# Performance work log

Measured on AMD Instinct MI355X. Metric: run time of the kernel, lower is better.

Reference implementation:

```python
import jax, jax.numpy as jnp
import numpy as np
from jax.ops import segment_sum

N = 100_000     # num nodes
E = 1_600_000   # num edges
G = 1024        # num graphs in batch
DIN, H, EMB, L = 128, 128, 64, 3
EPS = 1e-5


def setup_inputs() -> dict:
    key = jax.random.key(0)
    ks = jax.random.split(key, 12)
    x = jax.random.normal(ks[0], (N, DIN), dtype=jnp.float32)
    edge_index = jax.random.randint(ks[1], (2, E), 0, N, dtype=jnp.int32)
    batch = jnp.sort(jax.random.randint(ks[2], (N,), 0, G, dtype=jnp.int32))
    s = 0.05
    W_in = jax.random.normal(ks[3], (DIN, H), dtype=jnp.float32) * s
    b_in = jnp.zeros((H,), dtype=jnp.float32)
    Ws = jax.random.normal(ks[4], (L, H, H), dtype=jnp.float32) * s
    bs = jnp.zeros((L, H), dtype=jnp.float32)
    gammas = jnp.ones((L, H), dtype=jnp.float32)
    betas = jnp.zeros((L, H), dtype=jnp.float32)
    W1 = jax.random.normal(ks[5], (H, H), dtype=jnp.float32) * s
    b1 = jnp.zeros((H,), dtype=jnp.float32)
    W2 = jax.random.normal(ks[6], (H, EMB), dtype=jnp.float32) * s
    b2 = jnp.zeros((EMB,), dtype=jnp.float32)
    return {"x": x, "edge_index": edge_index, "batch": batch,
            "W_in": W_in, "b_in": b_in, "Ws": Ws, "bs": bs,
            "gammas": gammas, "betas": betas,
            "W1": W1, "b1": b1, "W2": W2, "b2": b2}


def reference(x, edge_index, batch, W_in, b_in, Ws, bs, gammas, betas, W1, b1, W2, b2):
    src, dst = edge_index[0], edge_index[1]
    # GCN normalization with implicit self-loops: deg = in-degree + 1
    deg = segment_sum(jnp.ones((E,), x.dtype), dst, num_segments=N) + 1.0
    dinv = jax.lax.rsqrt(deg)                      # deg^{-1/2}, [N]
    edge_norm = (dinv[src] * dinv[dst])[:, None]   # [E,1]
    self_norm = (dinv * dinv)[:, None]             # [N,1] = 1/deg

    h = jax.nn.relu(x @ W_in + b_in)               # input projection (dropout=0 / eval)
    for i in range(L):
        hw = h @ Ws[i]                             # [N,H] linear transform
        agg = segment_sum(hw[src] * edge_norm, dst, num_segments=N)
        h = agg + hw * self_norm + bs[i]           # GCNConv output (self-loop term fused)
        # BatchNorm1d over node dim (training-mode batch statistics)
        mean = jnp.mean(h, axis=0)
        var = jnp.var(h, axis=0)
        h = (h - mean) * jax.lax.rsqrt(var + EPS) * gammas[i] + betas[i]
        h = jax.nn.relu(h)

    # global mean pool per graph
    cnt = segment_sum(jnp.ones((N,), x.dtype), batch, num_segments=G)
    pooled = segment_sum(h, batch, num_segments=G) / jnp.maximum(cnt, 1.0)[:, None]

    out = jax.nn.relu(pooled @ W1 + b1) @ W2 + b2  # [G, EMB]
    return out
```

## Files before the change

### kernel.cpp

```cpp
#include <hip/hip_runtime.h>

#define HD 128
#define EMB 64
#define EPS 1e-5f

__device__ __forceinline__ float4 ld4(const float* p) {
    return *reinterpret_cast<const float4*>(p);
}

__device__ __forceinline__ unsigned short f2bf(float f) {
    unsigned u = __float_as_uint(f);
    u += 0x7FFF + ((u >> 16) & 1);
    return (unsigned short)(u >> 16);
}
__device__ __forceinline__ float bf2f(unsigned short b) {
    return __uint_as_float((unsigned)b << 16);
}
__device__ __forceinline__ float blo(unsigned u) { return __uint_as_float(u << 16); }
__device__ __forceinline__ float bhi(unsigned u) { return __uint_as_float(u & 0xffff0000u); }

__global__ void k_hist(const int* __restrict__ dst, int* __restrict__ deg, int e) {
    int i = blockIdx.x * blockDim.x + threadIdx.x;
    if (i < e) atomicAdd(&deg[dst[i]], 1);
}

__global__ void k_dinv(const int* __restrict__ deg, float* __restrict__ dinv, int n) {
    int i = blockIdx.x * blockDim.x + threadIdx.x;
    if (i < n) dinv[i] = 1.0f / sqrtf((float)deg[i] + 1.0f);
}

__global__ void k_scan_part(const int* __restrict__ deg, int* __restrict__ out,
                            int* __restrict__ bsum, int n) {
    __shared__ int s[256];
    int i = blockIdx.x * 256 + threadIdx.x;
    int v = (i < n) ? deg[i] : 0;
    s[threadIdx.x] = v;
    __syncthreads();
    #pragma unroll
    for (int off = 1; off < 256; off <<= 1) {
        int t = (threadIdx.x >= off) ? s[threadIdx.x - off] : 0;
        __syncthreads();
        s[threadIdx.x] += t;
        __syncthreads();
    }
    if (i < n) out[i] = s[threadIdx.x] - v;
    if (threadIdx.x == 255) bsum[blockIdx.x] = s[255];
}

__global__ void k_scan_mid(int* __restrict__ bsum, int nb) {
    __shared__ int s[512];
    int t = threadIdx.x;
    int v = (t < nb) ? bsum[t] : 0;
    s[t] = v;
    __syncthreads();
    for (int off = 1; off < 512; off <<= 1) {
        int u = (t >= off) ? s[t - off] : 0;
        __syncthreads();
        s[t] += u;
        __syncthreads();
    }
    if (t < nb) bsum[t] = s[t] - v;
}

__global__ void k_scan_add(int* __restrict__ rs, const int* __restrict__ bsum,
                           int n, int e_total) {
    int i = blockIdx.x * 256 + threadIdx.x;
    if (i < n) rs[i] += bsum[blockIdx.x];
    if (i == 0) rs[n] = e_total;
}

__global__ void k_scatter(const int* __restrict__ src, const int* __restrict__ dst,
                          int* __restrict__ cursor, int* __restrict__ csr_src, int e) {
    int i = blockIdx.x * blockDim.x + threadIdx.x;
    if (i < e) {
        int d = dst[i];
        int pos = atomicAdd(&cursor[d], 1);
        csr_src[pos] = src[i];
    }
}

template <bool APPLY_BN, bool OUT_BIAS_RELU, bool OUT_BF16>
__global__ void k_gemm(const float* __restrict__ A, const float* __restrict__ W,
                       const float* __restrict__ bias,
                       const float* __restrict__ aff_a, const float* __restrict__ aff_b,
                       void* __restrict__ Cout, int M) {
    __shared__ float As[32][64];
    __shared__ float Bs[32][128];
    const int tid = threadIdx.x;
    const int tx = tid & 31;
    const int ty = tid >> 5;
    const int row0 = blockIdx.x * 64;

    float acc[8][4];
    #pragma unroll
    for (int i = 0; i < 8; ++i)
        #pragma unroll
        for (int j = 0; j < 4; ++j) acc[i][j] = 0.0f;

    for (int k0 = 0; k0 < HD; k0 += 32) {
        #pragma unroll
        for (int it = 0; it < 2; ++it) {
            int idx = tid + it * 256;
            int m = idx >> 3;
            int k4 = (idx & 7) << 2;
            int gm = row0 + m;
            float4 v = make_float4(0.f, 0.f, 0.f, 0.f);
            if (gm < M) v = ld4(A + (size_t)gm * HD + k0 + k4);
            if (APPLY_BN) {
                float4 a4 = ld4(aff_a + k0 + k4);
                float4 b4 = ld4(aff_b + k0 + k4);
                v.x = fmaxf(fmaf(v.x, a4.x, b4.x), 0.f);
                v.y = fmaxf(fmaf(v.y, a4.y, b4.y), 0.f);
                v.z = fmaxf(fmaf(v.z, a4.z, b4.z), 0.f);
                v.w = fmaxf(fmaf(v.w, a4.w, b4.w), 0.f);
            }
            As[k4 + 0][m] = v.x; As[k4 + 1][m] = v.y;
            As[k4 + 2][m] = v.z; As[k4 + 3][m] = v.w;
        }
        #pragma unroll
        for (int it = 0; it < 4; ++it) {
            int idx = tid + it * 256;
            int kk = idx >> 5;
            int n4 = (idx & 31) << 2;
            *reinterpret_cast<float4*>(&Bs[kk][n4]) = ld4(W + (size_t)(k0 + kk) * HD + n4);
        }
        __syncthreads();
        #pragma unroll
        for (int k = 0; k < 32; ++k) {
            float4 b4 = *reinterpret_cast<const float4*>(&Bs[k][tx * 4]);
            float4 a0 = *reinterpret_cast<const float4*>(&As[k][ty * 8]);
            float4 a1 = *reinterpret_cast<const float4*>(&As[k][ty * 8 + 4]);
            float a[8] = {a0.x, a0.y, a0.z, a0.w, a1.x, a1.y, a1.z, a1.w};
            float b[4] = {b4.x, b4.y, b4.z, b4.w};
            #pragma unroll
            for (int i = 0; i < 8; ++i)
                #pragma unroll
                for (int j = 0; j < 4; ++j)
                    acc[i][j] = fmaf(a[i], b[j], acc[i][j]);
        }
        __syncthreads();
    }
    #pragma unroll
    for (int i = 0; i < 8; ++i) {
        int gm = row0 + ty * 8 + i;
        if (gm < M) {
            float4 o = make_float4(acc[i][0], acc[i][1], acc[i][2], acc[i][3]);
            if (OUT_BIAS_RELU) {
                float4 bb = ld4(bias + tx * 4);
                o.x = fmaxf(o.x + bb.x, 0.f);
                o.y = fmaxf(o.y + bb.y, 0.f);
                o.z = fmaxf(o.z + bb.z, 0.f);
                o.w = fmaxf(o.w + bb.w, 0.f);
            }
            if (OUT_BF16) {
                unsigned short b0 = f2bf(o.x), b1 = f2bf(o.y),
                               b2 = f2bf(o.z), b3 = f2bf(o.w);
                uint2 pk;
                pk.x = (unsigned)b0 | ((unsigned)b1 << 16);
                pk.y = (unsigned)b2 | ((unsigned)b3 << 16);
                *reinterpret_cast<uint2*>((unsigned short*)Cout + (size_t)gm * HD + tx * 4) = pk;
            } else {
                *reinterpret_cast<float4*>((float*)Cout + (size_t)gm * HD + tx * 4) = o;
            }
        }
    }
}

#define NPB 8
__global__ void k_agg(const unsigned short* __restrict__ hw, const int* __restrict__ row_start,
                      const int* __restrict__ csr_src, const float* __restrict__ dinv,
                      const float* __restrict__ bias_row, float* __restrict__ h_pre,
                      float* __restrict__ colsum, float* __restrict__ colsumsq, int n) {
    const int tid  = threadIdx.x;
    const int lane = tid & 63;
    const int slot = tid >> 6;
    const int q    = lane & 15;
    const int grp  = lane >> 4;
    const int n0 = blockIdx.x * (4 * NPB);
    const uint4* __restrict__ hw4 = (const uint4*)hw;

    float b8[8];
    #pragma unroll
    for (int k = 0; k < 8; ++k) b8[k] = bias_row[q * 8 + k];

    float psum8[8], psq8[8];
    #pragma unroll
    for (int k = 0; k < 8; ++k) { psum8[k] = 0.f; psq8[k] = 0.f; }

    for (int nn = 0; nn < NPB; ++nn) {
        int node = n0 + nn * 4 + slot;
        if (node >= n) continue;
        float dn = dinv[node];
        float acc[8];
        #pragma unroll
        for (int k = 0; k < 8; ++k) acc[k] = 0.f;

        const int jb = row_start[node], je = row_start[node + 1];
        for (int j = jb; j < je; j += 8) {
            int e0 = j + grp;
            int s0 = (e0 < je) ? csr_src[e0] : 0;
            float w0 = (e0 < je) ? dinv[s0] * dn : 0.f;
            uint4 r0 = hw4[(size_t)s0 * 16 + q];
            int e1 = j + 4 + grp;
            int s1 = (e1 < je) ? csr_src[e1] : 0;
            float w1 = (e1 < je) ? dinv[s1] * dn : 0.f;
            uint4 r1 = hw4[(size_t)s1 * 16 + q];

            acc[0] = fmaf(blo(r0.x), w0, acc[0]); acc[1] = fmaf(bhi(r0.x), w0, acc[1]);
            acc[2] = fmaf(blo(r0.y), w0, acc[2]); acc[3] = fmaf(bhi(r0.y), w0, acc[3]);
            acc[4] = fmaf(blo(r0.z), w0, acc[4]); acc[5] = fmaf(bhi(r0.z), w0, acc[5]);
            acc[6] = fmaf(blo(r0.w), w0, acc[6]); acc[7] = fmaf(bhi(r0.w), w0, acc[7]);

            acc[0] = fmaf(blo(r1.x), w1, acc[0]); acc[1] = fmaf(bhi(r1.x), w1, acc[1]);
            acc[2] = fmaf(blo(r1.y), w1, acc[2]); acc[3] = fmaf(bhi(r1.y), w1, acc[3]);
            acc[4] = fmaf(blo(r1.z), w1, acc[4]); acc[5] = fmaf(bhi(r1.z), w1, acc[5]);
            acc[6] = fmaf(blo(r1.w), w1, acc[6]); acc[7] = fmaf(bhi(r1.w), w1, acc[7]);
        }

        #pragma unroll
        for (int k = 0; k < 8; ++k) acc[k] += __shfl_xor(acc[k], 16, 64);
        #pragma unroll
        for (int k = 0; k < 8; ++k) acc[k] += __shfl_xor(acc[k], 32, 64);

        uint4 ow = hw4[(size_t)node * 16 + q];
        float sn = dn * dn;
        acc[0] = fmaf(blo(ow.x), sn, acc[0] + b8[0]);
        acc[1] = fmaf(bhi(ow.x), sn, acc[1] + b8[1]);
        acc[2] = fmaf(blo(ow.y), sn, acc[2] + b8[2]);
        acc[3] = fmaf(bhi(ow.y), sn, acc[3] + b8[3]);
        acc[4] = fmaf(blo(ow.z), sn, acc[4] + b8[4]);
        acc[5] = fmaf(bhi(ow.z), sn, acc[5] + b8[5]);
        acc[6] = fmaf(blo(ow.w), sn, acc[6] + b8[6]);
        acc[7] = fmaf(bhi(ow.w), sn, acc[7] + b8[7]);

        if (grp == 0) {
            float* dst = h_pre + (size_t)node * HD + q * 8;
            *reinterpret_cast<float4*>(dst)     = make_float4(acc[0], acc[1], acc[2], acc[3]);
            *reinterpret_cast<float4*>(dst + 4) = make_float4(acc[4], acc[5], acc[6], acc[7]);
            #pragma unroll
            for (int k = 0; k < 8; ++k) {
                psum8[k] += acc[k];
                psq8[k] = fmaf(acc[k], acc[k], psq8[k]);
            }
        }
    }

    __shared__ float redS[4][128];
    __shared__ float redQ[4][128];
    if (grp == 0) {
        #pragma unroll
        for (int k = 0; k < 8; ++k) {
            redS[slot][q * 8 + k] = psum8[k];
            redQ[slot][q * 8 + k] = psq8[k];
        }
    }
    __syncthreads();
    int f = tid & 127;
    if (tid < 128) {
        float s = redS[0][f] + redS[1][f] + redS[2][f] + redS[3][f];
        atomicAdd(&colsum[f], s);
    } else {
        float s = redQ[0][f] + redQ[1][f] + redQ[2][f] + redQ[3][f];
        atomicAdd(&colsumsq[f], s);
    }
}

__global__ void k_bncoef(float* __restrict__ colsum, float* __restrict__ colsumsq,
                         const float* __restrict__ gamma, const float* __restrict__ beta,
                         float* __restrict__ aff_a, float* __restrict__ aff_b, int n) {
    int f = threadIdx.x;
    float inv_n = 1.0f / (float)n;
    float mean = colsum[f] * inv_n;
    float var = colsumsq[f] * inv_n - mean * mean;
    float rstd = 1.0f / sqrtf(var + EPS);
    float a = gamma[f] * rstd;
    aff_a[f] = a;
    aff_b[f] = beta[f] - mean * a;
    colsum[f] = 0.f;
    colsumsq[f] = 0.f;
}

__global__ void k_gbounds(const int* __restrict__ batch, int* __restrict__ gstart,
                          int n, int g) {
    int gi = blockIdx.x * blockDim.x + threadIdx.x;
    if (gi > g) return;
    int lo = 0, hi = n;
    while (lo < hi) {
        int mid = (lo + hi) >> 1;
        if (batch[mid] < gi) lo = mid + 1; else hi = mid;
    }
    gstart[gi] = lo;
}

__global__ void k_pool(const float* __restrict__ h_pre, const int* __restrict__ gstart,
                       const float* __restrict__ aff_a, const float* __restrict__ aff_b,
                       float* __restrict__ pooled) {
    const int gi = blockIdx.x;
    const int tid = threadIdx.x;
    const int lane = tid & 63;
    const int half = tid >> 6;
    const float2* __restrict__ h2 = (const float2*)h_pre;
    const float2 a2 = *((const float2*)aff_a + lane);
    const float2 b2 = *((const float2*)aff_b + lane);
    int s = gstart[gi], e = gstart[gi + 1];
    float2 sum = make_float2(0.f, 0.f);
    for (int i = s + half; i < e; i += 2) {
        float2 v = h2[(size_t)i * 64 + lane];
        sum.x += fmaxf(fmaf(v.x, a2.x, b2.x), 0.f);
        sum.y += fmaxf(fmaf(v.y, a2.y, b2.y), 0.f);
    }
    __shared__ float2 red[128];
    red[tid] = sum;
    __syncthreads();
    if (half == 0) {
        float2 o = red[tid + 64];
        sum.x += o.x; sum.y += o.y;
        float inv = 1.0f / fmaxf((float)(e - s), 1.0f);
        float2* p2 = (float2*)pooled;
        p2[(size_t)gi * 64 + lane] = make_float2(sum.x * inv, sum.y * inv);
    }
}

__global__ void k_head(const float* __restrict__ pooled, const float* __restrict__ W1,
                       const float* __restrict__ b1, const float* __restrict__ W2,
                       const float* __restrict__ b2, float* __restrict__ out) {
    __shared__ float p[HD];
    __shared__ float t[HD];
    int gi = blockIdx.x;
    int j = threadIdx.x;
    p[j] = pooled[(size_t)gi * HD + j];
    __syncthreads();
    float acc = b1[j];
    #pragma unroll 8
    for (int k = 0; k < HD; ++k) acc = fmaf(p[k], W1[(size_t)k * HD + j], acc);
    t[j] = fmaxf(acc, 0.f);
    __syncthreads();
    if (j < EMB) {
        float o = b2[j];
        #pragma unroll 8
        for (int k = 0; k < HD; ++k) o = fmaf(t[k], W2[(size_t)k * EMB + j], o);
        out[(size_t)gi * EMB + j] = o;
    }
}

extern "C" void kernel_launch(void* const* d_in, const int* in_sizes, int n_in,
                              void* d_out, int out_size, void* d_ws, size_t ws_size,
                              hipStream_t stream) {
    const float* x     = (const float*)d_in[0];
    const int*   ei    = (const int*)d_in[1];
    const int*   batch = (const int*)d_in[2];
    const float* W_in  = (const float*)d_in[3];
    const float* b_in  = (const float*)d_in[4];
    const float* Ws    = (const float*)d_in[5];
    const float* bs    = (const float*)d_in[6];
    const float* gam   = (const float*)d_in[7];
    const float* bet   = (const float*)d_in[8];
    const float* W1    = (const float*)d_in[9];
    const float* b1    = (const float*)d_in[10];
    const float* W2    = (const float*)d_in[11];
    const float* b2    = (const float*)d_in[12];
    float* out = (float*)d_out;

    const int n = in_sizes[0] / HD;
    const int e = in_sizes[1] / 2;
    const int g = out_size / EMB;

    const int* esrc = ei;
    const int* edst = ei + e;

    char* w = (char*)d_ws;
    auto alloc = [&](size_t bytes) {
        char* p = w;
        w += (bytes + 255) & ~(size_t)255;
        return p;
    };
    float* hbuf             = (float*)alloc((size_t)n * HD * 4);
    unsigned short* hw      = (unsigned short*)alloc((size_t)n * HD * 2);
    int*   csr_src = (int*)alloc((size_t)e * 4);
    int*   deg     = (int*)alloc((size_t)n * 4);
    float* dinv    = (float*)alloc((size_t)n * 4);
    int*   rstart  = (int*)alloc((size_t)(n + 1) * 4);
    int*   cursor  = (int*)alloc((size_t)n * 4);
    int*   bsum    = (int*)alloc(512 * 4);
    float* colsum  = (float*)alloc(256 * 4);
    float* colsumsq = colsum + HD;
    float* aff_a   = (float*)alloc(256 * 4);
    float* aff_b   = aff_a + HD;
    int*   gstart  = (int*)alloc((size_t)(g + 1) * 4);
    float* pooled  = (float*)alloc((size_t)g * HD * 4);

    hipMemsetAsync(deg, 0, (size_t)n * 4, stream);
    hipMemsetAsync(colsum, 0, 256 * 4, stream);

    const int eb = (e + 255) / 256;
    const int nb = (n + 255) / 256;

    k_hist<<<eb, 256, 0, stream>>>(edst, deg, e);
    k_dinv<<<nb, 256, 0, stream>>>(deg, dinv, n);
    k_scan_part<<<nb, 256, 0, stream>>>(deg, rstart, bsum, n);
    k_scan_mid<<<1, 512, 0, stream>>>(bsum, nb);
    k_scan_add<<<nb, 256, 0, stream>>>(rstart, bsum, n, e);
    hipMemcpyAsync(cursor, rstart, (size_t)n * 4, hipMemcpyDeviceToDevice, stream);
    k_scatter<<<eb, 256, 0, stream>>>(esrc, edst, cursor, csr_src, e);

    const int gb = (n + 63) / 64;
    k_gemm<false, true, false><<<gb, 256, 0, stream>>>(x, W_in, b_in, nullptr, nullptr, hbuf, n);

    const int ab = (n + 4 * NPB - 1) / (4 * NPB);
    for (int i = 0; i < 3; ++i) {
        if (i == 0)
            k_gemm<false, false, true><<<gb, 256, 0, stream>>>(
                hbuf, Ws + (size_t)i * HD * HD, nullptr, nullptr, nullptr, hw, n);
        else
            k_gemm<true, false, true><<<gb, 256, 0, stream>>>(
                hbuf, Ws + (size_t)i * HD * HD, nullptr, aff_a, aff_b, hw, n);
        k_agg<<<ab, 256, 0, stream>>>(hw, rstart, csr_src, dinv, bs + (size_t)i * HD,
                                      hbuf, colsum, colsumsq, n);
        k_bncoef<<<1, HD, 0, stream>>>(colsum, colsumsq, gam + (size_t)i * HD,
                                       bet + (size_t)i * HD, aff_a, aff_b, n);
    }

    k_gbounds<<<(g + 256) / 256, 256, 0, stream>>>(batch, gstart, n, g);
    k_pool<<<g, 128, 0, stream>>>(hbuf, gstart, aff_a, aff_b, pooled);
    k_head<<<g, HD, 0, stream>>>(pooled, W1, b1, W2, b2, out);
}
```

Measured before the change: 945.8 us.

## Replace FP32 SIMT GEMM with bf16 MFMA using pre-transposed bf16 weights

Rewrites the dense node GEMMs to use MFMA 16x16x32 bf16 instructions. The weights are transposed and converted to bf16 once by a new prep kernel, then staged with the activations in XOR-swizzled shared memory to avoid bank conflicts. The goal is to cut the FP32 FMA compute of the four N x 128 x 128 GEMMs. In exchange, inputs and weights are rounded to bf16, including the first projection of x, which lowers precision. Output stores become scalar 2- or 4-byte writes instead of vectorized ones.

```diff
diff --git a/kernel.cpp b/kernel.cpp
--- a/kernel.cpp
+++ b/kernel.cpp
@@ -3,6 +3,9 @@
 #define HD 128
 #define EMB 64
 #define EPS 1e-5f
+
+typedef __bf16 bf16x8 __attribute__((ext_vector_type(8)));
+typedef float f32x4 __attribute__((ext_vector_type(4)));
 
 __device__ __forceinline__ float4 ld4(const float* p) {
     return *reinterpret_cast<const float4*>(p);
@@ -18,6 +21,9 @@
 }
 __device__ __forceinline__ float blo(unsigned u) { return __uint_as_float(u << 16); }
 __device__ __forceinline__ float bhi(unsigned u) { return __uint_as_float(u & 0xffff0000u); }
+__device__ __forceinline__ unsigned pk2(float a, float b) {
+    return (unsigned)f2bf(a) | ((unsigned)f2bf(b) << 16);
+}
 
 __global__ void k_hist(const int* __restrict__ dst, int* __restrict__ deg, int e) {
     int i = blockIdx.x * blockDim.x + threadIdx.x;
@@ -79,88 +85,113 @@
     }
 }
 
+__global__ void k_wprep(const float* __restrict__ W_in, const float* __restrict__ Ws,
+                        unsigned short* __restrict__ wt) {
+    int m = blockIdx.x >> 7;
+    int nn = blockIdx.x & 127;
+    int k = threadIdx.x;
+    const float* src = (m == 0) ? W_in : Ws + (size_t)(m - 1) * 16384;
+    wt[(size_t)m * 16384 + nn * 128 + k] = f2bf(src[k * 128 + nn]);
+}
+
 template <bool APPLY_BN, bool OUT_BIAS_RELU, bool OUT_BF16>
-__global__ void k_gemm(const float* __restrict__ A, const float* __restrict__ W,
-                       const float* __restrict__ bias,
-                       const float* __restrict__ aff_a, const float* __restrict__ aff_b,
-                       void* __restrict__ Cout, int M) {
-    __shared__ float As[32][64];
-    __shared__ float Bs[32][128];
+__global__ __launch_bounds__(256) void k_gemm(
+        const float* __restrict__ A, const unsigned short* __restrict__ Wt,
+        const float* __restrict__ bias,
+        const float* __restrict__ aff_a, const float* __restrict__ aff_b,
+        void* __restrict__ Cout, int M) {
+    __shared__ char sA[64 * 256];
+    __shared__ char sB[128 * 256];
     const int tid = threadIdx.x;
-    const int tx = tid & 31;
-    const int ty = tid >> 5;
     const int row0 = blockIdx.x * 64;
 
-    float acc[8][4];
-    #pragma unroll
-    for (int i = 0; i < 8; ++i)
-        #pragma unroll
-        for (int j = 0; j < 4; ++j) acc[i][j] = 0.0f;
-
-    for (int k0 = 0; k0 < HD; k0 += 32) {
-        #pragma unroll
-        for (int it = 0; it < 2; ++it) {
-            int idx = tid + it * 256;
-            int m = idx >> 3;
-            int k4 = (idx & 7) << 2;
-            int gm = row0 + m;
-            float4 v = make_float4(0.f, 0.f, 0.f, 0.f);
-            if (gm < M) v = ld4(A + (size_t)gm * HD + k0 + k4);
-            if (APPLY_BN) {
-                float4 a4 = ld4(aff_a + k0 + k4);
-                float4 b4 = ld4(aff_b + k0 + k4);
-                v.x = fmaxf(fmaf(v.x, a4.x, b4.x), 0.f);
-                v.y = fmaxf(fmaf(v.y, a4.y, b4.y), 0.f);
-                v.z = fmaxf(fmaf(v.z, a4.z, b4.z), 0.f);
-                v.w = fmaxf(fmaf(v.w, a4.w, b4.w), 0.f);
+    #pragma unroll
+    for (int it = 0; it < 8; ++it) {
+        int idx = it * 256 + tid;
+        int r = idx >> 4, c = idx & 15;
+        uint4 v = reinterpret_cast<const uint4*>(Wt)[idx];
+        int byte = r * 256 + c * 16;
+        *reinterpret_cast<uint4*>(sB + (byte ^ ((r & 7) << 4))) = v;
+    }
+    #pragma unroll
+    for (int it = 0; it < 4; ++it) {
+        int idx = it * 256 + tid;
+        int r = idx >> 4, c = idx & 15;
+        int gm = row0 + r;
+        float4 v0 = make_float4(0.f, 0.f, 0.f, 0.f), v1 = v0;
+        if (gm < M) {
+            v0 = ld4(A + (size_t)gm * HD + c * 8);
+            v1 = ld4(A + (size_t)gm * HD + c * 8 + 4);
+        }
+        if (APPLY_BN) {
+            float4 a0 = ld4(aff_a + c * 8), a1 = ld4(aff_a + c * 8 + 4);
+            float4 b0 = ld4(aff_b + c * 8), b1 = ld4(aff_b + c * 8 + 4);
+            v0.x = fmaxf(fmaf(v0.x, a0.x, b0.x), 0.f);
+            v0.y = fmaxf(fmaf(v0.y, a0.y, b0.y), 0.f);
+            v0.z = fmaxf(fmaf(v0.z, a0.z, b0.z), 0.f);
+            v0.w = fmaxf(fmaf(v0.w, a0.w, b0.w), 0.f);
+            v1.x = fmaxf(fmaf(v1.x, a1.x, b1.x), 0.f);
+            v1.y = fmaxf(fmaf(v1.y, a1.y, b1.y), 0.f);
+            v1.z = fmaxf(fmaf(v1.z, a1.z, b1.z), 0.f);
+            v1.w = fmaxf(fmaf(v1.w, a1.w, b1.w), 0.f);
+        }
+        uint4 pk;
+        pk.x = pk2(v0.x, v0.y); pk.y = pk2(v0.z, v0.w);
+        pk.z = pk2(v1.x, v1.y); pk.w = pk2(v1.z, v1.w);
+        int byte = r * 256 + c * 16;
+        *reinterpret_cast<uint4*>(sA + (byte ^ ((r & 7) << 4))) = pk;
+    }
+    __syncthreads();
+
+    const int wave = tid >> 6;
+    const int lane = tid & 63;
+    const int l15 = lane & 15;
+    const int kq  = lane >> 4;
+
+    bf16x8 af[4];
+    {
+        int arow = wave * 16 + l15;
+        int base = arow * 256;
+        int sw = (arow & 7) << 4;
+        #pragma unroll
+        for (int ks = 0; ks < 4; ++ks) {
+            int byte = base + kq * 16 + ks * 64;
+            af[ks] = __builtin_bit_cast(bf16x8,
+                *reinterpret_cast<const uint4*>(sA + (byte ^ sw)));
+        }
+    }
+
+    #pragma unroll
+    for (int nt = 0; nt < 8; ++nt) {
+        int bcol = nt * 16 + l15;
+        int bbase = bcol * 256;
+        int bsw = (bcol & 7) << 4;
+        f32x4 c = {0.f, 0.f, 0.f, 0.f};
+        #pragma unroll
+        for (int ks = 0; ks < 4; ++ks) {
+            int byte = bbase + kq * 16 + ks * 64;
+            bf16x8 bf = __builtin_bit_cast(bf16x8,
+                *reinterpret_cast<const uint4*>(sB + (byte ^ bsw)));
+            c = __builtin_amdgcn_mfma_f32_16x16x32_bf16(af[ks], bf, c, 0, 0, 0);
+        }
+        int col = nt * 16 + l15;
+        int grbase = row0 + wave * 16 + kq * 4;
+        if (OUT_BF16) {
+            unsigned short* C16 = (unsigned short*)Cout;
+            #pragma unroll
+            for (int i = 0; i < 4; ++i) {
+                int gr = grbase + i;
+                if (gr < M) C16[(size_t)gr * HD + col] = f2bf(c[i]);
             }
-            As[k4 + 0][m] = v.x; As[k4 + 1][m] = v.y;
-            As[k4 + 2][m] = v.z; As[k4 + 3][m] = v.w;
-        }
-        #pragma unroll
-        for (int it = 0; it < 4; ++it) {
-            int idx = tid + it * 256;
-            int kk = idx >> 5;
-            int n4 = (idx & 31) << 2;
-            *reinterpret_cast<float4*>(&Bs[kk][n4]) = ld4(W + (size_t)(k0 + kk) * HD + n4);
-        }
-        __syncthreads();
-        #pragma unroll
-        for (int k = 0; k < 32; ++k) {
-            float4 b4 = *reinterpret_cast<const float4*>(&Bs[k][tx * 4]);
-            float4 a0 = *reinterpret_cast<const float4*>(&As[k][ty * 8]);
-            float4 a1 = *reinterpret_cast<const float4*>(&As[k][ty * 8 + 4]);
-            float a[8] = {a0.x, a0.y, a0.z, a0.w, a1.x, a1.y, a1.z, a1.w};
-            float b[4] = {b4.x, b4.y, b4.z, b4.w};
+        } else {
+            float* C32 = (float*)Cout;
+            float bb = OUT_BIAS_RELU ? bias[col] : 0.f;
             #pragma unroll
-            for (int i = 0; i < 8; ++i)
-                #pragma unroll
-                for (int j = 0; j < 4; ++j)
-                    acc[i][j] = fmaf(a[i], b[j], acc[i][j]);
-        }
-        __syncthreads();
-    }
-    #pragma unroll
-    for (int i = 0; i < 8; ++i) {
-        int gm = row0 + ty * 8 + i;
-        if (gm < M) {
-            float4 o = make_float4(acc[i][0], acc[i][1], acc[i][2], acc[i][3]);
-            if (OUT_BIAS_RELU) {
-                float4 bb = ld4(bias + tx * 4);
-                o.x = fmaxf(o.x + bb.x, 0.f);
-                o.y = fmaxf(o.y + bb.y, 0.f);
-                o.z = fmaxf(o.z + bb.z, 0.f);
-                o.w = fmaxf(o.w + bb.w, 0.f);
-            }
-            if (OUT_BF16) {
-                unsigned short b0 = f2bf(o.x), b1 = f2bf(o.y),
-                               b2 = f2bf(o.z), b3 = f2bf(o.w);
-                uint2 pk;
-                pk.x = (unsigned)b0 | ((unsigned)b1 << 16);
-                pk.y = (unsigned)b2 | ((unsigned)b3 << 16);
-                *reinterpret_cast<uint2*>((unsigned short*)Cout + (size_t)gm * HD + tx * 4) = pk;
-            } else {
-                *reinterpret_cast<float4*>((float*)Cout + (size_t)gm * HD + tx * 4) = o;
+            for (int i = 0; i < 4; ++i) {
+                int gr = grbase + i;
+                float o = c[i];
+                if (OUT_BIAS_RELU) o = fmaxf(o + bb, 0.f);
+                if (gr < M) C32[(size_t)gr * HD + col] = o;
             }
         }
     }
@@ -376,6 +407,7 @@
     };
     float* hbuf             = (float*)alloc((size_t)n * HD * 4);
     unsigned short* hw      = (unsigned short*)alloc((size_t)n * HD * 2);
+    unsigned short* wtbuf   = (unsigned short*)alloc((size_t)4 * HD * HD * 2);
     int*   csr_src = (int*)alloc((size_t)e * 4);
     int*   deg     = (int*)alloc((size_t)n * 4);
     float* dinv    = (float*)alloc((size_t)n * 4);
@@ -395,6 +427,7 @@
     const int eb = (e + 255) / 256;
     const int nb = (n + 255) / 256;
 
+    k_wprep<<<512, 128, 0, stream>>>(W_in, Ws, wtbuf);
     k_hist<<<eb, 256, 0, stream>>>(edst, deg, e);
     k_dinv<<<nb, 256, 0, stream>>>(deg, dinv, n);
     k_scan_part<<<nb, 256, 0, stream>>>(deg, rstart, bsum, n);
@@ -404,16 +437,17 @@
     k_scatter<<<eb, 256, 0, stream>>>(esrc, edst, cursor, csr_src, e);
 
     const int gb = (n + 63) / 64;
-    k_gemm<false, true, false><<<gb, 256, 0, stream>>>(x, W_in, b_in, nullptr, nullptr, hbuf, n);
+    k_gemm<false, true, false><<<gb, 256, 0, stream>>>(
+        x, wtbuf, b_in, nullptr, nullptr, hbuf, n);
 
     const int ab = (n + 4 * NPB - 1) / (4 * NPB);
     for (int i = 0; i < 3; ++i) {
         if (i == 0)
             k_gemm<false, false, true><<<gb, 256, 0, stream>>>(
-                hbuf, Ws + (size_t)i * HD * HD, nullptr, nullptr, nullptr, hw, n);
+                hbuf, wtbuf + (size_t)(i + 1) * HD * HD, nullptr, nullptr, nullptr, hw, n);
         else
             k_gemm<true, false, true><<<gb, 256, 0, stream>>>(
-                hbuf, Ws + (size_t)i * HD * HD, nullptr, aff_a, aff_b, hw, n);
+                hbuf, wtbuf + (size_t)(i + 1) * HD * HD, nullptr, aff_a, aff_b, hw, n);
         k_agg<<<ab, 256, 0, stream>>>(hw, rstart, csr_src, dinv, bs + (size_t)i * HD,
                                       hbuf, colsum, colsumsq, n);
         k_bncoef<<<1, HD, 0, stream>>>(colsum, colsumsq, gam + (size_t)i * HD,
```

After: 837.7 us. -11.4%, faster.
